# Performance work log

Hardware: AMD Instinct MI355X
Metric: run time of the kernel (lower is better)

## Reference

```python
import jax, jax.numpy as jnp
import numpy as np

D_IN = 1024
D_OUT = 1024
SEQ = 4096


def setup_inputs() -> dict:
    key = jax.random.key(0)
    k0, k1, k2, k3 = jax.random.split(key, 4)
    inputs = jax.random.normal(k0, (SEQ, D_IN), dtype=jnp.float32)
    # original uses torch.rand (uniform [0,1)) for weights
    W_q = jax.random.uniform(k1, (D_IN, D_OUT), dtype=jnp.float32)
    W_k = jax.random.uniform(k2, (D_IN, D_OUT), dtype=jnp.float32)
    W_v = jax.random.uniform(k3, (D_IN, D_OUT), dtype=jnp.float32)
    return {"inputs": inputs, "W_q": W_q, "W_k": W_k, "W_v": W_v}


def reference(inputs, W_q, W_k, W_v):
    queries = inputs @ W_q            # [S, d_out]
    keys = inputs @ W_k               # [S, d_out]
    values = inputs @ W_v             # [S, d_out]
    d_k = keys.shape[-1]
    scale = 1.0 / jnp.sqrt(jnp.asarray(d_k, dtype=queries.dtype))
    attn_scores = queries @ keys.T    # [S, S]
    attn_weights = jax.nn.softmax(attn_scores * scale, axis=-1)
    context_vectors = attn_weights @ values  # [S, d_out]
    return context_vectors
```

## Files before the change

kernel.cpp:

```cpp
#include <hip/hip_runtime.h>

typedef unsigned short u16;
typedef __attribute__((ext_vector_type(8))) short bf16x8;
typedef __attribute__((ext_vector_type(4))) float f32x4;

#define SEQ 4096
#define DIM 1024

__device__ __forceinline__ u16 f2bf(float f) {
  unsigned u = __float_as_uint(f);
  return (u16)((u + 0x7fffu + ((u >> 16) & 1u)) >> 16);
}
__device__ __forceinline__ float bf2f(u16 h) {
  return __uint_as_float(((unsigned)h) << 16);
}

__device__ __forceinline__ void gload_lds16(const void* g, void* l) {
  __builtin_amdgcn_global_load_lds(
      (const __attribute__((address_space(1))) void*)g,
      (__attribute__((address_space(3))) void*)l, 16, 0, 0);
}

#define VM0 asm volatile("s_waitcnt vmcnt(0)" ::: "memory")
#define VM2 asm volatile("s_waitcnt vmcnt(2)" ::: "memory")
#define VM4 asm volatile("s_waitcnt vmcnt(4)" ::: "memory")
#define VM6 asm volatile("s_waitcnt vmcnt(6)" ::: "memory")
#define BAR __builtin_amdgcn_s_barrier()

__device__ __forceinline__ size_t pkoff(int row, int col, int kd) {
  int tile = (row >> 7) * (kd >> 5) + (col >> 5);
  int r7 = row & 127, c5 = col & 31;
  int slot = ((r7 >> 4) << 6) | ((c5 >> 3) << 4) | (r7 & 15);
  return (size_t)tile * 4096 + (size_t)(slot * 8 + (c5 & 7));
}

__device__ __forceinline__ void stage_tile_pk(const u16* __restrict__ g,
                                              u16* lds, int tid) {
  const int w = tid >> 6;
  gload_lds16(g + (size_t)tid * 8, lds + (size_t)(w * 64) * 8);
  gload_lds16(g + (size_t)(256 + tid) * 8, lds + (size_t)(256 + w * 64) * 8);
}

__device__ __forceinline__ void stage_q512(const u16* __restrict__ g,
                                           int kb, int nkb, u16* ldsq, int tid) {
  const int w = tid >> 6;
  gload_lds16(g + (size_t)kb * 4096 + tid * 8, ldsq + w * 512);
  gload_lds16(g + ((size_t)nkb + kb) * 4096 + tid * 8, ldsq + 4096 + w * 512);
}

__device__ __forceinline__ void gemm3_256(
    const u16* __restrict__ A0, const u16* __restrict__ A1,
    const u16* __restrict__ B0, const u16* __restrict__ B1,
    int nkb, u16* lds, f32x4 (&acc)[8][4]) {
  const int tid = threadIdx.x;
  const int w = tid >> 6, l = tid & 63;
  const int wm = w >> 2, wn = w & 3;

#pragma unroll
  for (int mi = 0; mi < 8; ++mi)
#pragma unroll
    for (int ni = 0; ni < 4; ++ni)
      acc[mi][ni] = (f32x4){0.f, 0.f, 0.f, 0.f};

  const int QA0 = 0, QA1 = 8192, QB0 = 16384, QB1 = 24576;
  const int aoff = wm * 4096 + l * 8;
  const int boff = ((wn & 2) >> 1) * 4096 + (wn & 1) * 2048 + l * 8;

  stage_q512(A0, 0, nkb, lds + QA0, tid);
  stage_q512(B0, 0, nkb, lds + QB0, tid);
  stage_q512(B1, 0, nkb, lds + QB1, tid);
  stage_q512(A1, 0, nkb, lds + QA1, tid);

  for (int kb = 0; kb < nkb; ++kb) {
    u16* cur = lds + (kb & 1) * 32768;
    u16* nxt = lds + ((kb + 1) & 1) * 32768;
    const bool pf = (kb + 1 < nkb);
    bf16x8 a0[8], b0[4];

    VM4;
    BAR;
    if (pf) {
      stage_q512(A0, kb + 1, nkb, nxt + QA0, tid);
      stage_q512(B0, kb + 1, nkb, nxt + QB0, tid);
    }
#pragma unroll
    for (int i = 0; i < 8; ++i) a0[i] = *(const bf16x8*)(cur + QA0 + aoff + i * 512);
#pragma unroll
    for (int i = 0; i < 4; ++i) b0[i] = *(const bf16x8*)(cur + QB0 + boff + i * 512);
    __builtin_amdgcn_s_setprio(1);
#pragma unroll
    for (int mi = 0; mi < 8; ++mi)
#pragma unroll
      for (int ni = 0; ni < 4; ++ni)
        acc[mi][ni] = __builtin_amdgcn_mfma_f32_16x16x32_bf16(
            a0[mi], b0[ni], acc[mi][ni], 0, 0, 0);
    __builtin_amdgcn_s_setprio(0);

    if (pf) { VM6; } else { VM2; }
    BAR;
    if (pf) stage_q512(B1, kb + 1, nkb, nxt + QB1, tid);
    {
      bf16x8 b1[4];
#pragma unroll
      for (int i = 0; i < 4; ++i) b1[i] = *(const bf16x8*)(cur + QB1 + boff + i * 512);
      __builtin_amdgcn_s_setprio(1);
#pragma unroll
      for (int mi = 0; mi < 8; ++mi)
#pragma unroll
        for (int ni = 0; ni < 4; ++ni)
          acc[mi][ni] = __builtin_amdgcn_mfma_f32_16x16x32_bf16(
              a0[mi], b1[ni], acc[mi][ni], 0, 0, 0);
      __builtin_amdgcn_s_setprio(0);
    }

    if (pf) { VM6; } else { VM0; }
    BAR;
    if (pf) stage_q512(A1, kb + 1, nkb, nxt + QA1, tid);
    {
      bf16x8 a1[8];
#pragma unroll
      for (int i = 0; i < 8; ++i) a1[i] = *(const bf16x8*)(cur + QA1 + aoff + i * 512);
      __builtin_amdgcn_s_setprio(1);
#pragma unroll
      for (int mi = 0; mi < 8; ++mi)
#pragma unroll
        for (int ni = 0; ni < 4; ++ni)
          acc[mi][ni] = __builtin_amdgcn_mfma_f32_16x16x32_bf16(
              a1[mi], b0[ni], acc[mi][ni], 0, 0, 0);
      __builtin_amdgcn_s_setprio(0);
    }
  }
  __syncthreads();
}

__device__ __forceinline__ void gemm3_db(
    const u16* A0, const u16* A1, const u16* B0, const u16* B1,
    int nkb, u16* lds, f32x4 (&acc)[4][4]) {
  const int tid = threadIdx.x;
  const int w = tid >> 6, l = tid & 63;
  const int wm = w >> 1, wn = w & 1;

#pragma unroll
  for (int mi = 0; mi < 4; ++mi)
#pragma unroll
    for (int ni = 0; ni < 4; ++ni)
      acc[mi][ni] = (f32x4){0.f, 0.f, 0.f, 0.f};

  const int ao = wm * 2048 + l * 8;
  const int bo = wn * 2048 + l * 8;

  stage_tile_pk(A0, lds, tid);
  stage_tile_pk(B0, lds + 4096, tid);
  stage_tile_pk(A1, lds + 8192, tid);
  stage_tile_pk(B1, lds + 12288, tid);

  for (int kb = 0; kb < nkb; ++kb) {
    __syncthreads();
    if (kb + 1 < nkb) {
      u16* nb = lds + ((kb + 1) & 1) * 16384;
      const size_t off = (size_t)(kb + 1) * 4096;
      stage_tile_pk(A0 + off, nb, tid);
      stage_tile_pk(B0 + off, nb + 4096, tid);
      stage_tile_pk(A1 + off, nb + 8192, tid);
      stage_tile_pk(B1 + off, nb + 12288, tid);
    }
    const u16* cb = lds + (kb & 1) * 16384;
    const u16* lA0 = cb;
    const u16* lB0 = cb + 4096;
    const u16* lA1 = cb + 8192;
    const u16* lB1 = cb + 12288;

    bf16x8 a0[4], b0[4];
#pragma unroll
    for (int i = 0; i < 4; ++i) {
      a0[i] = *(const bf16x8*)(lA0 + ao + i * 512);
      b0[i] = *(const bf16x8*)(lB0 + bo + i * 512);
    }
#pragma unroll
    for (int mi = 0; mi < 4; ++mi)
#pragma unroll
      for (int ni = 0; ni < 4; ++ni)
        acc[mi][ni] = __builtin_amdgcn_mfma_f32_16x16x32_bf16(
            a0[mi], b0[ni], acc[mi][ni], 0, 0, 0);
    bf16x8 b1[4];
#pragma unroll
    for (int i = 0; i < 4; ++i) b1[i] = *(const bf16x8*)(lB1 + bo + i * 512);
#pragma unroll
    for (int mi = 0; mi < 4; ++mi)
#pragma unroll
      for (int ni = 0; ni < 4; ++ni)
        acc[mi][ni] = __builtin_amdgcn_mfma_f32_16x16x32_bf16(
            a0[mi], b1[ni], acc[mi][ni], 0, 0, 0);
    bf16x8 a1[4];
#pragma unroll
    for (int i = 0; i < 4; ++i) a1[i] = *(const bf16x8*)(lA1 + ao + i * 512);
#pragma unroll
    for (int mi = 0; mi < 4; ++mi)
#pragma unroll
      for (int ni = 0; ni < 4; ++ni)
        acc[mi][ni] = __builtin_amdgcn_mfma_f32_16x16x32_bf16(
            a1[mi], b0[ni], acc[mi][ni], 0, 0, 0);
  }
  __syncthreads();
}

__device__ __forceinline__ void gemm1_db(
    const u16* A, const u16* B, int nkb, u16* lds, f32x4 (&acc)[4][4]) {
  const int tid = threadIdx.x;
  const int w = tid >> 6, l = tid & 63;
  const int wm = w >> 1, wn = w & 1;

#pragma unroll
  for (int mi = 0; mi < 4; ++mi)
#pragma unroll
    for (int ni = 0; ni < 4; ++ni)
      acc[mi][ni] = (f32x4){0.f, 0.f, 0.f, 0.f};

  const int ao = wm * 2048 + l * 8;
  const int bo = wn * 2048 + l * 8;
  const int nit = nkb >> 1;

  stage_tile_pk(A, lds, tid);
  stage_tile_pk(A + 4096, lds + 4096, tid);
  stage_tile_pk(B, lds + 8192, tid);
  stage_tile_pk(B + 4096, lds + 12288, tid);

  for (int it = 0; it < nit; ++it) {
    __syncthreads();
    if (it + 1 < nit) {
      u16* nb = lds + ((it + 1) & 1) * 16384;
      const size_t off = (size_t)(it + 1) * 8192;
      stage_tile_pk(A + off, nb, tid);
      stage_tile_pk(A + off + 4096, nb + 4096, tid);
      stage_tile_pk(B + off, nb + 8192, tid);
      stage_tile_pk(B + off + 4096, nb + 12288, tid);
    }
    const u16* cb = lds + (it & 1) * 16384;
#pragma unroll
    for (int ht = 0; ht < 2; ++ht) {
      bf16x8 av[4], bv[4];
#pragma unroll
      for (int i = 0; i < 4; ++i) {
        av[i] = *(const bf16x8*)(cb + ht * 4096 + ao + i * 512);
        bv[i] = *(const bf16x8*)(cb + 8192 + ht * 4096 + bo + i * 512);
      }
#pragma unroll
      for (int mi = 0; mi < 4; ++mi)
#pragma unroll
        for (int ni = 0; ni < 4; ++ni)
          acc[mi][ni] = __builtin_amdgcn_mfma_f32_16x16x32_bf16(
              av[mi], bv[ni], acc[mi][ni], 0, 0, 0);
    }
  }
  __syncthreads();
}

#define EPILOGUE_IDX                                          \
  const int tid = threadIdx.x, w = tid >> 6, l = tid & 63;    \
  const int wm = w >> 1, wn = w & 1, lr = l & 15, q = l >> 4; \
  (void)tid;

__device__ __forceinline__ void epilogue_pack(
    f32x4 (&acc)[4][4], u16* lds, int row0, int col0, int kd,
    u16* __restrict__ H, u16* __restrict__ L) {
  const int tid = threadIdx.x, w = tid >> 6, l = tid & 63;
  const int wm = w >> 1, wn = w & 1, lr = l & 15, q = l >> 4;
  float* lC = (float*)lds;
#pragma unroll
  for (int hh = 0; hh < 2; ++hh) {
    if (wm == hh) {
#pragma unroll
      for (int mi = 0; mi < 4; ++mi)
#pragma unroll
        for (int ni = 0; ni < 4; ++ni)
#pragma unroll
          for (int r = 0; r < 4; ++r)
            lC[(mi * 16 + q * 4 + r) * 132 + wn * 64 + ni * 16 + lr] =
                acc[mi][ni][r];
    }
    __syncthreads();
#pragma unroll
    for (int j = 0; j < 2; ++j) {
      int c = tid + 256 * j;
      int row = c >> 3, c0 = (c & 7) * 16;
      u16 hbuf[16], lbuf[16];
#pragma unroll
      for (int i = 0; i < 16; ++i) {
        float v = lC[row * 132 + c0 + i];
        u16 hv = f2bf(v);
        hbuf[i] = hv;
        lbuf[i] = f2bf(v - bf2f(hv));
      }
      int rg = row0 + hh * 64 + row;
      size_t o0 = pkoff(rg, col0 + c0, kd);
      size_t o1 = pkoff(rg, col0 + c0 + 8, kd);
      *(bf16x8*)(H + o0) = *(bf16x8*)(hbuf);
      *(bf16x8*)(H + o1) = *(bf16x8*)(hbuf + 8);
      if (L) {
        *(bf16x8*)(L + o0) = *(bf16x8*)(lbuf);
        *(bf16x8*)(L + o1) = *(bf16x8*)(lbuf + 8);
      }
    }
    if (hh == 0) __syncthreads();
  }
}


__global__ __launch_bounds__(256) void prep_kernel(
    const float* __restrict__ X,
    const float* __restrict__ W0, const float* __restrict__ W1, const float* __restrict__ W2,
    u16* __restrict__ Xh, u16* __restrict__ Xl,
    u16* __restrict__ H0, u16* __restrict__ L0,
    u16* __restrict__ H1, u16* __restrict__ L1,
    u16* __restrict__ H2) {
  const int z = blockIdx.z;
  const int tx = threadIdx.x, ty = threadIdx.y;
  if (z == 0) {
    int idx = (blockIdx.y * 32 + blockIdx.x) * 256 + ty * 32 + tx;
    int row = idx >> 6;
    int c0 = (idx & 63) * 16;
    u16 h[16], lo[16];
#pragma unroll
    for (int j = 0; j < 4; ++j) {
      float4 x = *(const float4*)(X + (size_t)row * DIM + c0 + j * 4);
      float v;
      v = x.x; h[j*4+0] = f2bf(v); lo[j*4+0] = f2bf(v - bf2f(h[j*4+0]));
      v = x.y; h[j*4+1] = f2bf(v); lo[j*4+1] = f2bf(v - bf2f(h[j*4+1]));
      v = x.z; h[j*4+2] = f2bf(v); lo[j*4+2] = f2bf(v - bf2f(h[j*4+2]));
      v = x.w; h[j*4+3] = f2bf(v); lo[j*4+3] = f2bf(v - bf2f(h[j*4+3]));
    }
    size_t o0 = pkoff(row, c0, DIM);
    size_t o1 = pkoff(row, c0 + 8, DIM);
    *(bf16x8*)(Xh + o0) = *(bf16x8*)(h);
    *(bf16x8*)(Xl + o0) = *(bf16x8*)(lo);
    *(bf16x8*)(Xh + o1) = *(bf16x8*)(h + 8);
    *(bf16x8*)(Xl + o1) = *(bf16x8*)(lo + 8);
    return;
  }
  __shared__ float t[32][33];
  const float* W = (z == 1) ? W0 : (z == 2) ? W1 : W2;
  u16* H = (z == 1) ? H0 : (z == 2) ? H1 : H2;
  u16* L = (z == 1) ? L0 : (z == 2) ? L1 : nullptr;
  const int i0 = blockIdx.y * 32, o0 = blockIdx.x * 32;
#pragma unroll
  for (int m = 0; m < 4; ++m)
    t[ty + 8 * m][tx] = W[(size_t)(i0 + ty + 8 * m) * DIM + o0 + tx];
  __syncthreads();
#pragma unroll
  for (int m = 0; m < 4; ++m) {
    float v = t[tx][ty + 8 * m];
    u16 h = f2bf(v);
    size_t o = pkoff(o0 + ty + 8 * m, i0 + tx, DIM);
    H[o] = h;
    if (L) L[o] = f2bf(v - bf2f(h));
  }
}

__global__ __launch_bounds__(256) void qkv_kernel(
    const u16* __restrict__ Xh, const u16* __restrict__ Xl,
    const u16* __restrict__ Wh0, const u16* __restrict__ Wl0,
    const u16* __restrict__ Wh1, const u16* __restrict__ Wl1,
    const u16* __restrict__ Wh2,
    u16* __restrict__ Qh, u16* __restrict__ Ql,
    u16* __restrict__ Kh, u16* __restrict__ Kl,
    u16* __restrict__ VT) {
  __shared__ __align__(16) u16 lds[2 * 4 * 4096];
  const int z = blockIdx.z;
  const int bid = blockIdx.y * 8 + blockIdx.x;
  const int xcd = bid & 7, c = bid >> 3;
  const int Y = xcd * 4 + (c >> 3);
  const int X = c & 7;
  f32x4 acc[4][4];
  if (z < 2) {
    const u16* Wh = z ? Wh1 : Wh0;
    const u16* Wl = z ? Wl1 : Wl0;
    const int row0 = Y * 128, col0 = X * 128;
    gemm3_db(Xh + (size_t)row0 * DIM, Xl + (size_t)row0 * DIM,
             Wh + (size_t)col0 * DIM, Wl + (size_t)col0 * DIM,
             DIM / 32, lds, acc);
    epilogue_pack(acc, lds, row0, col0, DIM, z ? Kh : Qh, z ? Kl : Ql);
  } else {
    const int row0 = X * 128;
    const int col0 = Y * 128;
    gemm1_db(Wh2 + (size_t)row0 * DIM, Xh + (size_t)col0 * DIM,
             DIM / 32, lds, acc);
    epilogue_pack(acc, lds, row0, col0, SEQ, VT, nullptr);
  }
}

__global__ __launch_bounds__(512, 2) void s_kernel(
    const u16* __restrict__ Qh, const u16* __restrict__ Ql,
    const u16* __restrict__ Kh, const u16* __restrict__ Kl,
    float* __restrict__ S) {
  __shared__ __align__(16) u16 lds[2 * 32768];
  const int bid = blockIdx.y * 16 + blockIdx.x;
  const int xcd = bid & 7, c = bid >> 3;
  const int Y = (xcd & 3) * 4 + (c >> 3);
  const int X = (xcd >> 2) * 8 + (c & 7);
  const int row0 = Y * 256, col0 = X * 256;
  f32x4 acc[8][4];
  gemm3_256(Qh + (size_t)row0 * DIM, Ql + (size_t)row0 * DIM,
            Kh + (size_t)col0 * DIM, Kl + (size_t)col0 * DIM,
            DIM / 32, lds, acc);
  const int tid = threadIdx.x, w = tid >> 6, l = tid & 63;
  const int wm = w >> 2, wn = w & 3, lr = l & 15, q = l >> 4;
  const float scale = 0.03125f;
#pragma unroll
  for (int mi = 0; mi < 8; ++mi)
#pragma unroll
    for (int ni = 0; ni < 4; ++ni)
#pragma unroll
      for (int r = 0; r < 4; ++r) {
        int row = row0 + wm * 128 + mi * 16 + q * 4 + r;
        int col = col0 + wn * 64 + ni * 16 + lr;
        S[(size_t)row * SEQ + col] = acc[mi][ni][r] * scale;
      }
}

__global__ __launch_bounds__(256) void softmax_kernel(const float* __restrict__ S,
                                                      u16* __restrict__ P) {
  const int row = blockIdx.x;
  const float* s = S + (size_t)row * SEQ;
  const int tid = threadIdx.x;
  const int c0 = tid * 16;
  float v[16];
  float mx = -3.4e38f;
#pragma unroll
  for (int j = 0; j < 4; ++j) {
    float4 x = *(const float4*)(s + c0 + j * 4);
    v[j * 4 + 0] = x.x; v[j * 4 + 1] = x.y; v[j * 4 + 2] = x.z; v[j * 4 + 3] = x.w;
    mx = fmaxf(mx, fmaxf(fmaxf(x.x, x.y), fmaxf(x.z, x.w)));
  }
#pragma unroll
  for (int off = 32; off; off >>= 1) mx = fmaxf(mx, __shfl_xor(mx, off));
  __shared__ float red[8];
  const int w = tid >> 6, l = tid & 63;
  if (l == 0) red[w] = mx;
  __syncthreads();
  mx = fmaxf(fmaxf(red[0], red[1]), fmaxf(red[2], red[3]));
  float sum = 0.f;
#pragma unroll
  for (int i = 0; i < 16; ++i) {
    v[i] = __expf(v[i] - mx);
    sum += v[i];
  }
#pragma unroll
  for (int off = 32; off; off >>= 1) sum += __shfl_xor(sum, off);
  if (l == 0) red[4 + w] = sum;
  __syncthreads();
  sum = red[4] + red[5] + red[6] + red[7];
  const float inv = 1.f / sum;
  u16 p[16];
#pragma unroll
  for (int i = 0; i < 16; ++i) p[i] = f2bf(v[i] * inv);
  *(bf16x8*)(P + pkoff(row, c0, SEQ)) = *(bf16x8*)(p);
  *(bf16x8*)(P + pkoff(row, c0 + 8, SEQ)) = *(bf16x8*)(p + 8);
}

__global__ __launch_bounds__(256) void o_kernel(const u16* __restrict__ P,
                                                const u16* __restrict__ VT,
                                                float* __restrict__ Opart) {
  __shared__ __align__(16) u16 lds[2 * 4 * 4096];
  const int z = blockIdx.z;
  const int bid = blockIdx.y * 8 + blockIdx.x;
  const int xcd = bid & 7, c = bid >> 3;
  const int Y = xcd * 4 + (c >> 3);
  const int X = c & 7;
  const int row0 = Y * 128, col0 = X * 128;
  const u16* A = P + (size_t)row0 * SEQ + (size_t)z * 64 * 4096;
  const u16* B = VT + (size_t)col0 * SEQ + (size_t)z * 64 * 4096;
  f32x4 acc[4][4];
  gemm1_db(A, B, 64, lds, acc);
  EPILOGUE_IDX
  float* O = Opart + (size_t)z * SEQ * DIM;
#pragma unroll
  for (int mi = 0; mi < 4; ++mi)
#pragma unroll
    for (int ni = 0; ni < 4; ++ni)
#pragma unroll
      for (int r = 0; r < 4; ++r) {
        int row = row0 + wm * 64 + mi * 16 + q * 4 + r;
        int col = col0 + wn * 64 + ni * 16 + lr;
        O[(size_t)row * DIM + col] = acc[mi][ni][r];
      }
}

__global__ __launch_bounds__(256) void o_reduce_kernel(const float* __restrict__ Op,
                                                       float* __restrict__ O) {
  const size_t N = (size_t)SEQ * DIM;
  size_t i = ((size_t)blockIdx.x * 256 + threadIdx.x) * 4;
  float4 a = *(const float4*)(Op + i);
  float4 b = *(const float4*)(Op + N + i);
  float4 rr;
  rr.x = a.x + b.x;
  rr.y = a.y + b.y;
  rr.z = a.z + b.z;
  rr.w = a.w + b.w;
  *(float4*)(O + i) = rr;
}

extern "C" void kernel_launch(void* const* d_in, const int* in_sizes, int n_in,
                              void* d_out, int out_size, void* d_ws, size_t ws_size,
                              hipStream_t stream) {
  const float* X = (const float*)d_in[0];
  const float* Wq = (const float*)d_in[1];
  const float* Wk = (const float*)d_in[2];
  const float* Wv = (const float*)d_in[3];

  const size_t MB = 1024 * 1024;
  char* w = (char*)d_ws;
  u16* Xh = (u16*)(w + 0 * MB);
  u16* Xl = (u16*)(w + 8 * MB);
  u16* WqhT = (u16*)(w + 16 * MB);
  u16* WqlT = (u16*)(w + 18 * MB);
  u16* WkhT = (u16*)(w + 20 * MB);
  u16* WklT = (u16*)(w + 22 * MB);
  u16* WvhT = (u16*)(w + 24 * MB);
  u16* Qh = (u16*)(w + 26 * MB);
  u16* Ql = (u16*)(w + 34 * MB);
  u16* Kh = (u16*)(w + 42 * MB);
  u16* Kl = (u16*)(w + 50 * MB);
  u16* VT = (u16*)(w + 58 * MB);
  float* S = (float*)(w + 66 * MB);
  u16* P = (u16*)(w + 26 * MB);
  float* Opart = (float*)(w + 66 * MB);

  prep_kernel<<<dim3(32, 32, 4), dim3(32, 8), 0, stream>>>(
      X, Wq, Wk, Wv, Xh, Xl, WqhT, WqlT, WkhT, WklT, WvhT);
  qkv_kernel<<<dim3(DIM / 128, SEQ / 128, 3), 256, 0, stream>>>(
      Xh, Xl, WqhT, WqlT, WkhT, WklT, WvhT, Qh, Ql, Kh, Kl, VT);
  s_kernel<<<dim3(SEQ / 256, SEQ / 256), 512, 0, stream>>>(Qh, Ql, Kh, Kl, S);
  softmax_kernel<<<SEQ, 256, 0, stream>>>(S, P);
  o_kernel<<<dim3(DIM / 128, SEQ / 128, 2), 256, 0, stream>>>(P, VT, Opart);
  o_reduce_kernel<<<(SEQ * DIM) / (256 * 4), 256, 0, stream>>>(Opart, (float*)d_out);
}
```

Measured before the change: 299.9 us.

## Move QKV projection to 256x256 tiles with 4-stage pipelined GEMM

The QKV projection kernel now uses 256x256 output tiles with 512 threads per block. The Q/K path reuses the existing gemm3_256 routine from the S kernel, and the V path gets a new gemm1_256 with a four-buffer, three-tile-deep global-to-LDS prefetch using explicit vmcnt waits. The epilogue is widened to match. This raises operand reuse per loaded tile and hides load latency better, but the grid shrinks from 768 to 192 blocks, which may leave compute units underfilled, and the XCD-aware block remapping is dropped.

New measurement: 308.4 us. 2.9% more time.

```diff
diff --git a/kernel.cpp b/kernel.cpp
--- a/kernel.cpp
+++ b/kernel.cpp
@@ -25,6 +25,7 @@
 #define VM2 asm volatile("s_waitcnt vmcnt(2)" ::: "memory")
 #define VM4 asm volatile("s_waitcnt vmcnt(4)" ::: "memory")
 #define VM6 asm volatile("s_waitcnt vmcnt(6)" ::: "memory")
+#define VM8 asm volatile("s_waitcnt vmcnt(8)" ::: "memory")
 #define BAR __builtin_amdgcn_s_barrier()
 
 __device__ __forceinline__ size_t pkoff(int row, int col, int kd) {
@@ -133,73 +134,51 @@
   __syncthreads();
 }
 
-__device__ __forceinline__ void gemm3_db(
-    const u16* A0, const u16* A1, const u16* B0, const u16* B1,
-    int nkb, u16* lds, f32x4 (&acc)[4][4]) {
+__device__ __forceinline__ void gemm1_256(
+    const u16* __restrict__ A, const u16* __restrict__ B,
+    int nkb, u16* lds, f32x4 (&acc)[8][4]) {
   const int tid = threadIdx.x;
   const int w = tid >> 6, l = tid & 63;
-  const int wm = w >> 1, wn = w & 1;
-
-#pragma unroll
-  for (int mi = 0; mi < 4; ++mi)
+  const int wm = w >> 2, wn = w & 3;
+
+#pragma unroll
+  for (int mi = 0; mi < 8; ++mi)
 #pragma unroll
     for (int ni = 0; ni < 4; ++ni)
       acc[mi][ni] = (f32x4){0.f, 0.f, 0.f, 0.f};
 
-  const int ao = wm * 2048 + l * 8;
-  const int bo = wn * 2048 + l * 8;
-
-  stage_tile_pk(A0, lds, tid);
-  stage_tile_pk(B0, lds + 4096, tid);
-  stage_tile_pk(A1, lds + 8192, tid);
-  stage_tile_pk(B1, lds + 12288, tid);
+  const int aoff = wm * 4096 + l * 8;
+  const int boff = ((wn & 2) >> 1) * 4096 + (wn & 1) * 2048 + l * 8;
+
+  stage_q512(A, 0, nkb, lds + 0 * 16384, tid);
+  stage_q512(B, 0, nkb, lds + 0 * 16384 + 8192, tid);
+  stage_q512(A, 1, nkb, lds + 1 * 16384, tid);
+  stage_q512(B, 1, nkb, lds + 1 * 16384 + 8192, tid);
+  stage_q512(A, 2, nkb, lds + 2 * 16384, tid);
+  stage_q512(B, 2, nkb, lds + 2 * 16384 + 8192, tid);
 
   for (int kb = 0; kb < nkb; ++kb) {
-    __syncthreads();
-    if (kb + 1 < nkb) {
-      u16* nb = lds + ((kb + 1) & 1) * 16384;
-      const size_t off = (size_t)(kb + 1) * 4096;
-      stage_tile_pk(A0 + off, nb, tid);
-      stage_tile_pk(B0 + off, nb + 4096, tid);
-      stage_tile_pk(A1 + off, nb + 8192, tid);
-      stage_tile_pk(B1 + off, nb + 12288, tid);
-    }
-    const u16* cb = lds + (kb & 1) * 16384;
-    const u16* lA0 = cb;
-    const u16* lB0 = cb + 4096;
-    const u16* lA1 = cb + 8192;
-    const u16* lB1 = cb + 12288;
-
-    bf16x8 a0[4], b0[4];
-#pragma unroll
-    for (int i = 0; i < 4; ++i) {
-      a0[i] = *(const bf16x8*)(lA0 + ao + i * 512);
-      b0[i] = *(const bf16x8*)(lB0 + bo + i * 512);
-    }
-#pragma unroll
-    for (int mi = 0; mi < 4; ++mi)
+    if (kb + 2 < nkb) { VM8; } else if (kb + 1 < nkb) { VM4; } else { VM0; }
+    BAR;
+    if (kb + 3 < nkb) {
+      u16* nb = lds + ((kb + 3) & 3) * 16384;
+      stage_q512(A, kb + 3, nkb, nb, tid);
+      stage_q512(B, kb + 3, nkb, nb + 8192, tid);
+    }
+    const u16* cb = lds + (kb & 3) * 16384;
+    bf16x8 av[8], bv[4];
+#pragma unroll
+    for (int i = 0; i < 8; ++i) av[i] = *(const bf16x8*)(cb + aoff + i * 512);
+#pragma unroll
+    for (int i = 0; i < 4; ++i) bv[i] = *(const bf16x8*)(cb + 8192 + boff + i * 512);
+    __builtin_amdgcn_s_setprio(1);
+#pragma unroll
+    for (int mi = 0; mi < 8; ++mi)
 #pragma unroll
       for (int ni = 0; ni < 4; ++ni)
         acc[mi][ni] = __builtin_amdgcn_mfma_f32_16x16x32_bf16(
-            a0[mi], b0[ni], acc[mi][ni], 0, 0, 0);
-    bf16x8 b1[4];
-#pragma unroll
-    for (int i = 0; i < 4; ++i) b1[i] = *(const bf16x8*)(lB1 + bo + i * 512);
-#pragma unroll
-    for (int mi = 0; mi < 4; ++mi)
-#pragma unroll
-      for (int ni = 0; ni < 4; ++ni)
-        acc[mi][ni] = __builtin_amdgcn_mfma_f32_16x16x32_bf16(
-            a0[mi], b1[ni], acc[mi][ni], 0, 0, 0);
-    bf16x8 a1[4];
-#pragma unroll
-    for (int i = 0; i < 4; ++i) a1[i] = *(const bf16x8*)(lA1 + ao + i * 512);
-#pragma unroll
-    for (int mi = 0; mi < 4; ++mi)
-#pragma unroll
-      for (int ni = 0; ni < 4; ++ni)
-        acc[mi][ni] = __builtin_amdgcn_mfma_f32_16x16x32_bf16(
-            a1[mi], b0[ni], acc[mi][ni], 0, 0, 0);
+            av[mi], bv[ni], acc[mi][ni], 0, 0, 0);
+    __builtin_amdgcn_s_setprio(0);
   }
   __syncthreads();
 }
@@ -260,38 +239,39 @@
   const int wm = w >> 1, wn = w & 1, lr = l & 15, q = l >> 4; \
   (void)tid;
 
-__device__ __forceinline__ void epilogue_pack(
-    f32x4 (&acc)[4][4], u16* lds, int row0, int col0, int kd,
+__device__ __forceinline__ void epilogue_pack256(
+    f32x4 (&acc)[8][4], u16* lds, int row0, int col0, int kd,
     u16* __restrict__ H, u16* __restrict__ L) {
   const int tid = threadIdx.x, w = tid >> 6, l = tid & 63;
-  const int wm = w >> 1, wn = w & 1, lr = l & 15, q = l >> 4;
+  const int wm = w >> 2, wn = w & 3, lr = l & 15, q = l >> 4;
   float* lC = (float*)lds;
 #pragma unroll
-  for (int hh = 0; hh < 2; ++hh) {
-    if (wm == hh) {
-#pragma unroll
-      for (int mi = 0; mi < 4; ++mi)
+  for (int p = 0; p < 4; ++p) {
+    if (wm == (p >> 1)) {
+      const int mib = (p & 1) * 4;
+#pragma unroll
+      for (int mi2 = 0; mi2 < 4; ++mi2)
 #pragma unroll
         for (int ni = 0; ni < 4; ++ni)
 #pragma unroll
           for (int r = 0; r < 4; ++r)
-            lC[(mi * 16 + q * 4 + r) * 132 + wn * 64 + ni * 16 + lr] =
-                acc[mi][ni][r];
+            lC[(mi2 * 16 + q * 4 + r) * 260 + wn * 64 + ni * 16 + lr] =
+                acc[mib + mi2][ni][r];
     }
     __syncthreads();
 #pragma unroll
     for (int j = 0; j < 2; ++j) {
-      int c = tid + 256 * j;
-      int row = c >> 3, c0 = (c & 7) * 16;
+      int u = tid + 512 * j;
+      int row = u >> 4, c0 = (u & 15) * 16;
       u16 hbuf[16], lbuf[16];
 #pragma unroll
       for (int i = 0; i < 16; ++i) {
-        float v = lC[row * 132 + c0 + i];
+        float v = lC[row * 260 + c0 + i];
         u16 hv = f2bf(v);
         hbuf[i] = hv;
         lbuf[i] = f2bf(v - bf2f(hv));
       }
-      int rg = row0 + hh * 64 + row;
+      int rg = row0 + p * 64 + row;
       size_t o0 = pkoff(rg, col0 + c0, kd);
       size_t o1 = pkoff(rg, col0 + c0 + 8, kd);
       *(bf16x8*)(H + o0) = *(bf16x8*)(hbuf);
@@ -301,7 +281,7 @@
         *(bf16x8*)(L + o1) = *(bf16x8*)(lbuf + 8);
       }
     }
-    if (hh == 0) __syncthreads();
+    if (p < 3) __syncthreads();
   }
 }
 
@@ -356,7 +336,7 @@
   }
 }
 
-__global__ __launch_bounds__(256) void qkv_kernel(
+__global__ __launch_bounds__(512, 2) void qkv_kernel(
     const u16* __restrict__ Xh, const u16* __restrict__ Xl,
     const u16* __restrict__ Wh0, const u16* __restrict__ Wl0,
     const u16* __restrict__ Wh1, const u16* __restrict__ Wl1,
@@ -364,27 +344,24 @@
     u16* __restrict__ Qh, u16* __restrict__ Ql,
     u16* __restrict__ Kh, u16* __restrict__ Kl,
     u16* __restrict__ VT) {
-  __shared__ __align__(16) u16 lds[2 * 4 * 4096];
+  __shared__ __align__(16) u16 lds[2 * 32768];
   const int z = blockIdx.z;
-  const int bid = blockIdx.y * 8 + blockIdx.x;
-  const int xcd = bid & 7, c = bid >> 3;
-  const int Y = xcd * 4 + (c >> 3);
-  const int X = c & 7;
-  f32x4 acc[4][4];
+  f32x4 acc[8][4];
   if (z < 2) {
     const u16* Wh = z ? Wh1 : Wh0;
     const u16* Wl = z ? Wl1 : Wl0;
-    const int row0 = Y * 128, col0 = X * 128;
-    gemm3_db(Xh + (size_t)row0 * DIM, Xl + (size_t)row0 * DIM,
-             Wh + (size_t)col0 * DIM, Wl + (size_t)col0 * DIM,
-             DIM / 32, lds, acc);
-    epilogue_pack(acc, lds, row0, col0, DIM, z ? Kh : Qh, z ? Kl : Ql);
+    const int row0 = blockIdx.y * 256;
+    const int col0 = blockIdx.x * 256;
+    gemm3_256(Xh + (size_t)row0 * DIM, Xl + (size_t)row0 * DIM,
+              Wh + (size_t)col0 * DIM, Wl + (size_t)col0 * DIM,
+              DIM / 32, lds, acc);
+    epilogue_pack256(acc, lds, row0, col0, DIM, z ? Kh : Qh, z ? Kl : Ql);
   } else {
-    const int row0 = X * 128;
-    const int col0 = Y * 128;
-    gemm1_db(Wh2 + (size_t)row0 * DIM, Xh + (size_t)col0 * DIM,
-             DIM / 32, lds, acc);
-    epilogue_pack(acc, lds, row0, col0, SEQ, VT, nullptr);
+    const int row0 = blockIdx.x * 256;
+    const int col0 = blockIdx.y * 256;
+    gemm1_256(Wh2 + (size_t)row0 * DIM, Xh + (size_t)col0 * DIM,
+              DIM / 32, lds, acc);
+    epilogue_pack256(acc, lds, row0, col0, SEQ, VT, nullptr);
   }
 }
 
@@ -527,7 +504,7 @@
 
   prep_kernel<<<dim3(32, 32, 4), dim3(32, 8), 0, stream>>>(
       X, Wq, Wk, Wv, Xh, Xl, WqhT, WqlT, WkhT, WklT, WvhT);
-  qkv_kernel<<<dim3(DIM / 128, SEQ / 128, 3), 256, 0, stream>>>(
+  qkv_kernel<<<dim3(DIM / 256, SEQ / 256, 3), 512, 0, stream>>>(
       Xh, Xl, WqhT, WqlT, WkhT, WklT, WvhT, Qh, Ql, Kh, Kl, VT);
   s_kernel<<<dim3(SEQ / 256, SEQ / 256), 512, 0, stream>>>(Qh, Ql, Kh, Kl, S);
   softmax_kernel<<<SEQ, 256, 0, stream>>>(S, P);
```
